# Kernel optimization log

Hardware: AMD Instinct MI355X
Metric: run time of the kernel (lower is better)

Reference implementation:

```python
import jax, jax.numpy as jnp
import numpy as np

B, S, H, D = 1, 2048, 16, 128
CAUSAL = True


def setup_inputs() -> dict:
    key = jax.random.key(0)
    kq, kk, kv = jax.random.split(key, 3)
    query = jax.random.normal(kq, (B, S, H, D), dtype=jnp.float32)
    k_ = jax.random.normal(kk, (B, S, H, D), dtype=jnp.float32)
    v_ = jax.random.normal(kv, (B, S, H, D), dtype=jnp.float32)
    return {"query": query, "key": k_, "value": v_}


def reference(query, key, value):
    # Single-device equivalent of LongContextAttention:
    # Ulysses all-to-all and ring pass are identity on one rank; the math is
    # standard scaled-dot-product attention with flash-attn's default scale
    # softmax_scale = 1/sqrt(head_dim) and causal masking.
    d = query.shape[-1]
    scale = 1.0 / jnp.sqrt(jnp.asarray(d, dtype=query.dtype))
    # [B,S,H,D] x [B,T,H,D] -> [B,H,S,T]
    scores = jnp.einsum("bshd,bthd->bhst", query, key) * scale
    if CAUSAL:
        s, t = scores.shape[-2], scores.shape[-1]
        mask = jnp.tril(jnp.ones((s, t), dtype=bool))
        scores = jnp.where(mask, scores, jnp.finfo(scores.dtype).min)
    probs = jax.nn.softmax(scores, axis=-1)
    out = jnp.einsum("bhst,bthd->bshd", probs, value)
    return out
```

## Files before the change

### kernel.cpp

```cpp
#include <hip/hip_runtime.h>
#include <hip/hip_bf16.h>
#include <math.h>

#define SS 2048
#define HH 16
#define DD 128
#define HD (HH*DD)
#define QBLK 64
#define KVBLK 64

typedef __attribute__((ext_vector_type(8))) short bf16x8;
typedef __attribute__((ext_vector_type(4))) float f32x4;

#if __has_builtin(__builtin_amdgcn_exp2f)
#define EXP2(x) __builtin_amdgcn_exp2f(x)
#else
#define EXP2(x) exp2f(x)
#endif

__device__ __forceinline__ ushort f2bf(float f) {
  __hip_bfloat16 h = __float2bfloat16(f);
  return __builtin_bit_cast(ushort, h);
}

__global__ __launch_bounds__(256, 2)
void attn_fwd(const float* __restrict__ Q, const float* __restrict__ K,
              const float* __restrict__ V, float* __restrict__ O) {
  __shared__ alignas(16) ushort Klds[KVBLK][136];
  __shared__ alignas(16) ushort VTlds[DD][72];
  __shared__ alignas(16) ushort Plds[4][16][72];

  const int tid  = threadIdx.x;
  const int lane = tid & 63;
  const int wid  = tid >> 6;
  const int n    = lane & 15;
  const int g    = lane >> 4;

  const int h  = blockIdx.x & (HH - 1);
  const int j  = blockIdx.x >> 4;
  const int qt = (j < 16) ? (31 - j) : (j - 16);
  const int qb = qt * QBLK;
  const int qw = qb + 16 * wid;

  const float SCALE = 1.44269504088896f / sqrtf((float)DD);

  bf16x8 qfrag[4];
  {
    const float* qrow = Q + ((size_t)(qw + n) * HH + h) * DD;
    #pragma unroll
    for (int ks = 0; ks < 4; ++ks) {
      const int d0 = 32 * ks + 8 * g;
      float4 x = *(const float4*)&qrow[d0];
      float4 y = *(const float4*)&qrow[d0 + 4];
      bf16x8 a;
      a[0] = (short)f2bf(x.x * SCALE); a[1] = (short)f2bf(x.y * SCALE);
      a[2] = (short)f2bf(x.z * SCALE); a[3] = (short)f2bf(x.w * SCALE);
      a[4] = (short)f2bf(y.x * SCALE); a[5] = (short)f2bf(y.y * SCALE);
      a[6] = (short)f2bf(y.z * SCALE); a[7] = (short)f2bf(y.w * SCALE);
      qfrag[ks] = a;
    }
  }

  f32x4 acc[8];
  #pragma unroll
  for (int d0 = 0; d0 < 8; ++d0) { acc[d0][0]=0.f; acc[d0][1]=0.f; acc[d0][2]=0.f; acc[d0][3]=0.f; }
  float m[4] = { -INFINITY, -INFINITY, -INFINITY, -INFINITY };
  float l[4] = { 0.f, 0.f, 0.f, 0.f };

  const float* Kbase = K + (size_t)h * DD;
  const float* Vbase = V + (size_t)h * DD;
  const int nt = qb / KVBLK + 1;

  float4 kreg[8];
  float4 vreg[8];

  {
    #pragma unroll
    for (int it = 0; it < 8; ++it) {
      int li = tid + it * 256;
      int t  = li >> 5;
      int c4 = (li & 31) << 2;
      kreg[it] = *(const float4*)&Kbase[(size_t)t * HD + c4];
    }
    const int dd0 = wid * 16 + n;
    #pragma unroll
    for (int half = 0; half < 2; ++half) {
      #pragma unroll
      for (int jj = 0; jj < 4; ++jj) {
        const float* vp = &Vbase[(size_t)(16 * jj + 4 * g) * HD + (dd0 + 64 * half)];
        vreg[half * 4 + jj] = make_float4(vp[0], vp[HD], vp[2 * HD], vp[3 * HD]);
      }
    }
  }

  for (int itile = 0; itile < nt; ++itile) {
    __syncthreads();

    #pragma unroll
    for (int it = 0; it < 8; ++it) {
      int li = tid + it * 256;
      int t  = li >> 5;
      int c4 = (li & 31) << 2;
      float4 x = kreg[it];
      ushort4 w;
      w.x = f2bf(x.x); w.y = f2bf(x.y); w.z = f2bf(x.z); w.w = f2bf(x.w);
      *(ushort4*)&Klds[t][c4] = w;
    }
    {
      const int dd0 = wid * 16 + n;
      #pragma unroll
      for (int half = 0; half < 2; ++half) {
        #pragma unroll
        for (int jj = 0; jj < 4; ++jj) {
          float4 x = vreg[half * 4 + jj];
          ushort4 w;
          w.x = f2bf(x.x); w.y = f2bf(x.y); w.z = f2bf(x.z); w.w = f2bf(x.w);
          *(ushort4*)&VTlds[dd0 + 64 * half][16 * jj + 4 * g] = w;
        }
      }
    }
    __syncthreads();

    if (itile + 1 < nt) {
      const int t0n = (itile + 1) * KVBLK;
      #pragma unroll
      for (int it = 0; it < 8; ++it) {
        int li = tid + it * 256;
        int t  = li >> 5;
        int c4 = (li & 31) << 2;
        kreg[it] = *(const float4*)&Kbase[(size_t)(t0n + t) * HD + c4];
      }
      const int dd0 = wid * 16 + n;
      #pragma unroll
      for (int half = 0; half < 2; ++half) {
        #pragma unroll
        for (int jj = 0; jj < 4; ++jj) {
          const float* vp = &Vbase[(size_t)(t0n + 16 * jj + 4 * g) * HD + (dd0 + 64 * half)];
          vreg[half * 4 + jj] = make_float4(vp[0], vp[HD], vp[2 * HD], vp[3 * HD]);
        }
      }
    }

    const int t0 = itile * KVBLK;

    f32x4 s[4];
    #pragma unroll
    for (int sub = 0; sub < 4; ++sub) { s[sub][0]=0.f; s[sub][1]=0.f; s[sub][2]=0.f; s[sub][3]=0.f; }
    #pragma unroll
    for (int ks = 0; ks < 4; ++ks) {
      #pragma unroll
      for (int sub = 0; sub < 4; ++sub) {
        bf16x8 b = *(const bf16x8*)&Klds[sub * 16 + n][32 * ks + 8 * g];
        s[sub] = __builtin_amdgcn_mfma_f32_16x16x32_bf16(qfrag[ks], b, s[sub], 0, 0, 0);
      }
    }

    if (t0 + KVBLK - 1 > qw) {
      #pragma unroll
      for (int sub = 0; sub < 4; ++sub) {
        int tg = t0 + sub * 16 + n;
        #pragma unroll
        for (int r = 0; r < 4; ++r) {
          int qg = qw + 4 * g + r;
          if (tg > qg) s[sub][r] = -INFINITY;
        }
      }
    }

    float mr[4];
    #pragma unroll
    for (int r = 0; r < 4; ++r)
      mr[r] = fmaxf(fmaxf(s[0][r], s[1][r]), fmaxf(s[2][r], s[3][r]));
    #pragma unroll
    for (int off = 1; off <= 8; off <<= 1) {
      #pragma unroll
      for (int r = 0; r < 4; ++r)
        mr[r] = fmaxf(mr[r], __shfl_xor(mr[r], off));
    }
    float corr[4];
    #pragma unroll
    for (int r = 0; r < 4; ++r) {
      float mn = fmaxf(m[r], mr[r]);
      corr[r] = EXP2(m[r] - mn);
      m[r] = mn;
    }
    float sr[4] = { 0.f, 0.f, 0.f, 0.f };
    #pragma unroll
    for (int sub = 0; sub < 4; ++sub) {
      #pragma unroll
      for (int r = 0; r < 4; ++r) {
        float p = EXP2(s[sub][r] - m[r]);
        sr[r] += p;
        Plds[wid][4 * g + r][sub * 16 + n] = f2bf(p);
      }
    }
    #pragma unroll
    for (int off = 1; off <= 8; off <<= 1) {
      #pragma unroll
      for (int r = 0; r < 4; ++r)
        sr[r] += __shfl_xor(sr[r], off);
    }
    #pragma unroll
    for (int r = 0; r < 4; ++r) l[r] = l[r] * corr[r] + sr[r];
    #pragma unroll
    for (int d0 = 0; d0 < 8; ++d0) {
      #pragma unroll
      for (int r = 0; r < 4; ++r) acc[d0][r] *= corr[r];
    }

    #pragma unroll
    for (int ks = 0; ks < 2; ++ks) {
      bf16x8 a = *(const bf16x8*)&Plds[wid][n][32 * ks + 8 * g];
      #pragma unroll
      for (int d0 = 0; d0 < 8; ++d0) {
        bf16x8 b = *(const bf16x8*)&VTlds[d0 * 16 + n][32 * ks + 8 * g];
        acc[d0] = __builtin_amdgcn_mfma_f32_16x16x32_bf16(a, b, acc[d0], 0, 0, 0);
      }
    }
  }

  float invl[4];
  #pragma unroll
  for (int r = 0; r < 4; ++r) invl[r] = 1.0f / l[r];
  #pragma unroll
  for (int d0 = 0; d0 < 8; ++d0) {
    #pragma unroll
    for (int r = 0; r < 4; ++r) {
      O[((size_t)(qw + 4 * g + r) * HH + h) * DD + d0 * 16 + n] = acc[d0][r] * invl[r];
    }
  }
}

extern "C" void kernel_launch(void* const* d_in, const int* in_sizes, int n_in,
                              void* d_out, int out_size, void* d_ws, size_t ws_size,
                              hipStream_t stream) {
  const float* Q = (const float*)d_in[0];
  const float* K = (const float*)d_in[1];
  const float* V = (const float*)d_in[2];
  float* O = (float*)d_out;
  dim3 grid((SS / QBLK) * HH);
  attn_fwd<<<grid, 256, 0, stream>>>(Q, K, V, O);
}
```

Before: 75.90 us.

## Split causal attention KV range into chunks with partial outputs and combine kernel

Splits each query tile's KV loop into chunks of at most 8 tiles, so the partial kernel runs more, shorter-lived blocks (1280 tasks) with more even load. Per-chunk unnormalized outputs, row max and row sum go to workspace, and a second kernel merges them with log-sum-exp weights. The goal is to cut the causal load-imbalance tail and raise occupancy, at the cost of a second launch and extra global traffic for the partial outputs. The exp2 intrinsic is also swapped for plain exp2f, and the old single kernel is kept as a fallback when the workspace is too small.

```diff
diff --git a/kernel.cpp b/kernel.cpp
--- a/kernel.cpp
+++ b/kernel.cpp
@@ -8,24 +8,24 @@
 #define HD (HH*DD)
 #define QBLK 64
 #define KVBLK 64
+#define CH 8
+#define NTASK_PER_H 80
+#define NTASK (NTASK_PER_H*HH)
 
 typedef __attribute__((ext_vector_type(8))) short bf16x8;
 typedef __attribute__((ext_vector_type(4))) float f32x4;
 
-#if __has_builtin(__builtin_amdgcn_exp2f)
-#define EXP2(x) __builtin_amdgcn_exp2f(x)
-#else
 #define EXP2(x) exp2f(x)
-#endif
 
 __device__ __forceinline__ ushort f2bf(float f) {
   __hip_bfloat16 h = __float2bfloat16(f);
   return __builtin_bit_cast(ushort, h);
 }
 
-__global__ __launch_bounds__(256, 2)
-void attn_fwd(const float* __restrict__ Q, const float* __restrict__ K,
-              const float* __restrict__ V, float* __restrict__ O) {
+__global__ __launch_bounds__(256, 3)
+void attn_partial(const float* __restrict__ Q, const float* __restrict__ K,
+                  const float* __restrict__ V, float* __restrict__ PO,
+                  float* __restrict__ PM, float* __restrict__ PL) {
   __shared__ alignas(16) ushort Klds[KVBLK][136];
   __shared__ alignas(16) ushort VTlds[DD][72];
   __shared__ alignas(16) ushort Plds[4][16][72];
@@ -36,11 +36,22 @@
   const int n    = lane & 15;
   const int g    = lane >> 4;
 
-  const int h  = blockIdx.x & (HH - 1);
-  const int j  = blockIdx.x >> 4;
-  const int qt = (j < 16) ? (31 - j) : (j - 16);
+  const int bx   = blockIdx.x;
+  const int h    = bx & 15;
+  const int task = bx >> 4;
+
+  int qt = 0, c = 0;
+  for (int q = 31; q >= 0; --q) {
+    int a = q >> 3, b = q & 7;
+    int base = q + 4 * a * (a - 1) + a * b;
+    if (task >= base) { qt = q; c = task - base; break; }
+  }
+
   const int qb = qt * QBLK;
   const int qw = qb + 16 * wid;
+  const int nt = qb / KVBLK + 1;
+  const int tile_lo = c * CH;
+  const int tile_hi = min(tile_lo + CH, nt);
 
   const float SCALE = 1.44269504088896f / sqrtf((float)DD);
 
@@ -69,31 +80,31 @@
 
   const float* Kbase = K + (size_t)h * DD;
   const float* Vbase = V + (size_t)h * DD;
-  const int nt = qb / KVBLK + 1;
 
   float4 kreg[8];
   float4 vreg[8];
 
   {
+    const int t0 = tile_lo * KVBLK;
     #pragma unroll
     for (int it = 0; it < 8; ++it) {
       int li = tid + it * 256;
       int t  = li >> 5;
       int c4 = (li & 31) << 2;
-      kreg[it] = *(const float4*)&Kbase[(size_t)t * HD + c4];
+      kreg[it] = *(const float4*)&Kbase[(size_t)(t0 + t) * HD + c4];
     }
     const int dd0 = wid * 16 + n;
     #pragma unroll
     for (int half = 0; half < 2; ++half) {
       #pragma unroll
       for (int jj = 0; jj < 4; ++jj) {
-        const float* vp = &Vbase[(size_t)(16 * jj + 4 * g) * HD + (dd0 + 64 * half)];
+        const float* vp = &Vbase[(size_t)(t0 + 16 * jj + 4 * g) * HD + (dd0 + 64 * half)];
         vreg[half * 4 + jj] = make_float4(vp[0], vp[HD], vp[2 * HD], vp[3 * HD]);
       }
     }
   }
 
-  for (int itile = 0; itile < nt; ++itile) {
+  for (int itile = tile_lo; itile < tile_hi; ++itile) {
     __syncthreads();
 
     #pragma unroll
@@ -121,7 +132,7 @@
     }
     __syncthreads();
 
-    if (itile + 1 < nt) {
+    if (itile + 1 < tile_hi) {
       const int t0n = (itile + 1) * KVBLK;
       #pragma unroll
       for (int it = 0; it < 8; ++it) {
@@ -219,6 +230,259 @@
     }
   }
 
+  float* po = PO + (size_t)bx * (QBLK * DD);
+  #pragma unroll
+  for (int d0 = 0; d0 < 8; ++d0) {
+    #pragma unroll
+    for (int r = 0; r < 4; ++r) {
+      po[(16 * wid + 4 * g + r) * DD + d0 * 16 + n] = acc[d0][r];
+    }
+  }
+  if (n == 0) {
+    #pragma unroll
+    for (int r = 0; r < 4; ++r) {
+      PM[(size_t)bx * QBLK + 16 * wid + 4 * g + r] = m[r];
+      PL[(size_t)bx * QBLK + 16 * wid + 4 * g + r] = l[r];
+    }
+  }
+}
+
+__global__ __launch_bounds__(256, 4)
+void attn_combine(const float* __restrict__ PO, const float* __restrict__ PM,
+                  const float* __restrict__ PL, float* __restrict__ O) {
+  const int bx = blockIdx.x;
+  const int h  = bx & 15;
+  const int qt = bx >> 4;
+  const int tid = threadIdx.x;
+  const int r  = tid >> 2;
+  const int d0 = (tid & 3) << 5;
+
+  const int a = qt >> 3, b = qt & 7;
+  const int base = qt + 4 * a * (a - 1) + a * b;
+  const int nc = a + 1;
+
+  float mc[4], lc[4];
+  float M = -INFINITY;
+  for (int cc = 0; cc < nc; ++cc) {
+    int pid = ((base + cc) << 4) | h;
+    mc[cc] = PM[(size_t)pid * QBLK + r];
+    lc[cc] = PL[(size_t)pid * QBLK + r];
+    M = fmaxf(M, mc[cc]);
+  }
+  float L = 0.f;
+  float4 o[8];
+  #pragma unroll
+  for (int k = 0; k < 8; ++k) o[k] = make_float4(0.f, 0.f, 0.f, 0.f);
+  for (int cc = 0; cc < nc; ++cc) {
+    int pid = ((base + cc) << 4) | h;
+    float w = EXP2(mc[cc] - M);
+    L += lc[cc] * w;
+    const float* po = PO + (size_t)pid * (QBLK * DD) + r * DD + d0;
+    #pragma unroll
+    for (int k = 0; k < 8; ++k) {
+      float4 x = *(const float4*)&po[4 * k];
+      o[k].x += x.x * w; o[k].y += x.y * w; o[k].z += x.z * w; o[k].w += x.w * w;
+    }
+  }
+  float inv = 1.0f / L;
+  float* op = O + ((size_t)(qt * QBLK + r) * HH + h) * DD + d0;
+  #pragma unroll
+  for (int k = 0; k < 8; ++k) {
+    float4 x = make_float4(o[k].x * inv, o[k].y * inv, o[k].z * inv, o[k].w * inv);
+    *(float4*)&op[4 * k] = x;
+  }
+}
+
+__global__ __launch_bounds__(256, 2)
+void attn_fwd(const float* __restrict__ Q, const float* __restrict__ K,
+              const float* __restrict__ V, float* __restrict__ O) {
+  __shared__ alignas(16) ushort Klds[KVBLK][136];
+  __shared__ alignas(16) ushort VTlds[DD][72];
+  __shared__ alignas(16) ushort Plds[4][16][72];
+
+  const int tid  = threadIdx.x;
+  const int lane = tid & 63;
+  const int wid  = tid >> 6;
+  const int n    = lane & 15;
+  const int g    = lane >> 4;
+
+  const int h  = blockIdx.x & (HH - 1);
+  const int j  = blockIdx.x >> 4;
+  const int qt = (j < 16) ? (31 - j) : (j - 16);
+  const int qb = qt * QBLK;
+  const int qw = qb + 16 * wid;
+
+  const float SCALE = 1.44269504088896f / sqrtf((float)DD);
+
+  bf16x8 qfrag[4];
+  {
+    const float* qrow = Q + ((size_t)(qw + n) * HH + h) * DD;
+    #pragma unroll
+    for (int ks = 0; ks < 4; ++ks) {
+      const int d0 = 32 * ks + 8 * g;
+      float4 x = *(const float4*)&qrow[d0];
+      float4 y = *(const float4*)&qrow[d0 + 4];
+      bf16x8 a;
+      a[0] = (short)f2bf(x.x * SCALE); a[1] = (short)f2bf(x.y * SCALE);
+      a[2] = (short)f2bf(x.z * SCALE); a[3] = (short)f2bf(x.w * SCALE);
+      a[4] = (short)f2bf(y.x * SCALE); a[5] = (short)f2bf(y.y * SCALE);
+      a[6] = (short)f2bf(y.z * SCALE); a[7] = (short)f2bf(y.w * SCALE);
+      qfrag[ks] = a;
+    }
+  }
+
+  f32x4 acc[8];
+  #pragma unroll
+  for (int d0 = 0; d0 < 8; ++d0) { acc[d0][0]=0.f; acc[d0][1]=0.f; acc[d0][2]=0.f; acc[d0][3]=0.f; }
+  float m[4] = { -INFINITY, -INFINITY, -INFINITY, -INFINITY };
+  float l[4] = { 0.f, 0.f, 0.f, 0.f };
+
+  const float* Kbase = K + (size_t)h * DD;
+  const float* Vbase = V + (size_t)h * DD;
+  const int nt = qb / KVBLK + 1;
+
+  float4 kreg[8];
+  float4 vreg[8];
+  {
+    #pragma unroll
+    for (int it = 0; it < 8; ++it) {
+      int li = tid + it * 256;
+      int t  = li >> 5;
+      int c4 = (li & 31) << 2;
+      kreg[it] = *(const float4*)&Kbase[(size_t)t * HD + c4];
+    }
+    const int dd0 = wid * 16 + n;
+    #pragma unroll
+    for (int half = 0; half < 2; ++half) {
+      #pragma unroll
+      for (int jj = 0; jj < 4; ++jj) {
+        const float* vp = &Vbase[(size_t)(16 * jj + 4 * g) * HD + (dd0 + 64 * half)];
+        vreg[half * 4 + jj] = make_float4(vp[0], vp[HD], vp[2 * HD], vp[3 * HD]);
+      }
+    }
+  }
+
+  for (int itile = 0; itile < nt; ++itile) {
+    __syncthreads();
+    #pragma unroll
+    for (int it = 0; it < 8; ++it) {
+      int li = tid + it * 256;
+      int t  = li >> 5;
+      int c4 = (li & 31) << 2;
+      float4 x = kreg[it];
+      ushort4 w;
+      w.x = f2bf(x.x); w.y = f2bf(x.y); w.z = f2bf(x.z); w.w = f2bf(x.w);
+      *(ushort4*)&Klds[t][c4] = w;
+    }
+    {
+      const int dd0 = wid * 16 + n;
+      #pragma unroll
+      for (int half = 0; half < 2; ++half) {
+        #pragma unroll
+        for (int jj = 0; jj < 4; ++jj) {
+          float4 x = vreg[half * 4 + jj];
+          ushort4 w;
+          w.x = f2bf(x.x); w.y = f2bf(x.y); w.z = f2bf(x.z); w.w = f2bf(x.w);
+          *(ushort4*)&VTlds[dd0 + 64 * half][16 * jj + 4 * g] = w;
+        }
+      }
+    }
+    __syncthreads();
+
+    if (itile + 1 < nt) {
+      const int t0n = (itile + 1) * KVBLK;
+      #pragma unroll
+      for (int it = 0; it < 8; ++it) {
+        int li = tid + it * 256;
+        int t  = li >> 5;
+        int c4 = (li & 31) << 2;
+        kreg[it] = *(const float4*)&Kbase[(size_t)(t0n + t) * HD + c4];
+      }
+      const int dd0 = wid * 16 + n;
+      #pragma unroll
+      for (int half = 0; half < 2; ++half) {
+        #pragma unroll
+        for (int jj = 0; jj < 4; ++jj) {
+          const float* vp = &Vbase[(size_t)(t0n + 16 * jj + 4 * g) * HD + (dd0 + 64 * half)];
+          vreg[half * 4 + jj] = make_float4(vp[0], vp[HD], vp[2 * HD], vp[3 * HD]);
+        }
+      }
+    }
+
+    const int t0 = itile * KVBLK;
+    f32x4 s[4];
+    #pragma unroll
+    for (int sub = 0; sub < 4; ++sub) { s[sub][0]=0.f; s[sub][1]=0.f; s[sub][2]=0.f; s[sub][3]=0.f; }
+    #pragma unroll
+    for (int ks = 0; ks < 4; ++ks) {
+      #pragma unroll
+      for (int sub = 0; sub < 4; ++sub) {
+        bf16x8 b = *(const bf16x8*)&Klds[sub * 16 + n][32 * ks + 8 * g];
+        s[sub] = __builtin_amdgcn_mfma_f32_16x16x32_bf16(qfrag[ks], b, s[sub], 0, 0, 0);
+      }
+    }
+    if (t0 + KVBLK - 1 > qw) {
+      #pragma unroll
+      for (int sub = 0; sub < 4; ++sub) {
+        int tg = t0 + sub * 16 + n;
+        #pragma unroll
+        for (int r = 0; r < 4; ++r) {
+          int qg = qw + 4 * g + r;
+          if (tg > qg) s[sub][r] = -INFINITY;
+        }
+      }
+    }
+    float mr[4];
+    #pragma unroll
+    for (int r = 0; r < 4; ++r)
+      mr[r] = fmaxf(fmaxf(s[0][r], s[1][r]), fmaxf(s[2][r], s[3][r]));
+    #pragma unroll
+    for (int off = 1; off <= 8; off <<= 1) {
+      #pragma unroll
+      for (int r = 0; r < 4; ++r)
+        mr[r] = fmaxf(mr[r], __shfl_xor(mr[r], off));
+    }
+    float corr[4];
+    #pragma unroll
+    for (int r = 0; r < 4; ++r) {
+      float mn = fmaxf(m[r], mr[r]);
+      corr[r] = EXP2(m[r] - mn);
+      m[r] = mn;
+    }
+    float sr[4] = { 0.f, 0.f, 0.f, 0.f };
+    #pragma unroll
+    for (int sub = 0; sub < 4; ++sub) {
+      #pragma unroll
+      for (int r = 0; r < 4; ++r) {
+        float p = EXP2(s[sub][r] - m[r]);
+        sr[r] += p;
+        Plds[wid][4 * g + r][sub * 16 + n] = f2bf(p);
+      }
+    }
+    #pragma unroll
+    for (int off = 1; off <= 8; off <<= 1) {
+      #pragma unroll
+      for (int r = 0; r < 4; ++r)
+        sr[r] += __shfl_xor(sr[r], off);
+    }
+    #pragma unroll
+    for (int r = 0; r < 4; ++r) l[r] = l[r] * corr[r] + sr[r];
+    #pragma unroll
+    for (int d0 = 0; d0 < 8; ++d0) {
+      #pragma unroll
+      for (int r = 0; r < 4; ++r) acc[d0][r] *= corr[r];
+    }
+    #pragma unroll
+    for (int ks = 0; ks < 2; ++ks) {
+      bf16x8 a = *(const bf16x8*)&Plds[wid][n][32 * ks + 8 * g];
+      #pragma unroll
+      for (int d0 = 0; d0 < 8; ++d0) {
+        bf16x8 b = *(const bf16x8*)&VTlds[d0 * 16 + n][32 * ks + 8 * g];
+        acc[d0] = __builtin_amdgcn_mfma_f32_16x16x32_bf16(a, b, acc[d0], 0, 0, 0);
+      }
+    }
+  }
+
   float invl[4];
   #pragma unroll
   for (int r = 0; r < 4; ++r) invl[r] = 1.0f / l[r];
@@ -238,6 +502,18 @@
   const float* K = (const float*)d_in[1];
   const float* V = (const float*)d_in[2];
   float* O = (float*)d_out;
-  dim3 grid((SS / QBLK) * HH);
-  attn_fwd<<<grid, 256, 0, stream>>>(Q, K, V, O);
+
+  const size_t po_elems = (size_t)NTASK * QBLK * DD;
+  const size_t ml_elems = (size_t)NTASK * QBLK;
+  const size_t ws_needed = (po_elems + 2 * ml_elems) * sizeof(float);
+
+  if (ws_size >= ws_needed) {
+    float* PO = (float*)d_ws;
+    float* PM = PO + po_elems;
+    float* PL = PM + ml_elems;
+    attn_partial<<<NTASK, 256, 0, stream>>>(Q, K, V, PO, PM, PL);
+    attn_combine<<<(SS / QBLK) * HH, 256, 0, stream>>>(PO, PM, PL, O);
+  } else {
+    attn_fwd<<<(SS / QBLK) * HH, 256, 0, stream>>>(Q, K, V, O);
+  }
 }
```

New measurement: 116.9 us. 1.54x slower.

## Precompute bf16 K and transposed V in a prep kernel, swizzle LDS

Applied to the files above, without the earlier changes.

Adds a prep kernel that converts K to bf16 and V to a transposed bf16 layout in workspace once per call. The attention kernel then streams half-size bf16 tiles with contiguous 16-byte loads instead of redoing the fp32 conversion and strided V gathers in every query block. LDS tiles lose their padding and use an XOR swizzle to avoid bank conflicts, and launch bounds rise to 3 blocks per CU. The cost is an extra kernel launch plus a workspace round trip. The exp2 macro is also switched from the amdgcn builtin to exp2f.

```diff
diff --git a/kernel.cpp b/kernel.cpp
--- a/kernel.cpp
+++ b/kernel.cpp
@@ -12,22 +12,73 @@
 typedef __attribute__((ext_vector_type(8))) short bf16x8;
 typedef __attribute__((ext_vector_type(4))) float f32x4;
 
-#if __has_builtin(__builtin_amdgcn_exp2f)
-#define EXP2(x) __builtin_amdgcn_exp2f(x)
-#else
 #define EXP2(x) exp2f(x)
-#endif
 
 __device__ __forceinline__ ushort f2bf(float f) {
   __hip_bfloat16 h = __float2bfloat16(f);
   return __builtin_bit_cast(ushort, h);
 }
 
-__global__ __launch_bounds__(256, 2)
-void attn_fwd(const float* __restrict__ Q, const float* __restrict__ K,
-              const float* __restrict__ V, float* __restrict__ O) {
-  __shared__ alignas(16) ushort Klds[KVBLK][136];
-  __shared__ alignas(16) ushort VTlds[DD][72];
+__global__ __launch_bounds__(256, 4)
+void prep_kv(const float* __restrict__ K, const float* __restrict__ V,
+             ushort* __restrict__ Kbf, ushort* __restrict__ VTg) {
+  __shared__ ushort Vlds[64][136];
+  const int tid = threadIdx.x;
+  const int h  = blockIdx.x & 15;
+  const int t0 = (blockIdx.x >> 4) * 64;
+
+  #pragma unroll
+  for (int j = 0; j < 2; ++j) {
+    int li = tid + j * 256;
+    int t  = li >> 3;
+    int c  = (li & 7) << 4;
+    const float* src = K + ((size_t)(t0 + t) * HH + h) * DD + c;
+    ushort tmp[16];
+    #pragma unroll
+    for (int q = 0; q < 4; ++q) {
+      float4 x = *(const float4*)(src + 4 * q);
+      tmp[4*q+0] = f2bf(x.x); tmp[4*q+1] = f2bf(x.y);
+      tmp[4*q+2] = f2bf(x.z); tmp[4*q+3] = f2bf(x.w);
+    }
+    ushort* dst = Kbf + ((size_t)h * SS + t0 + t) * DD + c;
+    *(uint4*)dst       = *(uint4*)&tmp[0];
+    *(uint4*)(dst + 8) = *(uint4*)&tmp[8];
+  }
+
+  #pragma unroll
+  for (int j = 0; j < 2; ++j) {
+    int li = tid + j * 256;
+    int t  = li >> 3;
+    int c  = (li & 7) << 4;
+    const float* src = V + ((size_t)(t0 + t) * HH + h) * DD + c;
+    #pragma unroll
+    for (int q = 0; q < 4; ++q) {
+      float4 x = *(const float4*)(src + 4 * q);
+      ushort4 w; w.x = f2bf(x.x); w.y = f2bf(x.y); w.z = f2bf(x.z); w.w = f2bf(x.w);
+      *(ushort4*)&Vlds[t][c + 4 * q] = w;
+    }
+  }
+  __syncthreads();
+
+  #pragma unroll
+  for (int j = 0; j < 2; ++j) {
+    int li  = tid + j * 256;
+    int d   = li >> 2;
+    int t16 = (li & 3) << 4;
+    ushort tmp[16];
+    #pragma unroll
+    for (int k = 0; k < 16; ++k) tmp[k] = Vlds[t16 + k][d];
+    ushort* dst = VTg + ((size_t)h * DD + d) * SS + t0 + t16;
+    *(uint4*)dst       = *(uint4*)&tmp[0];
+    *(uint4*)(dst + 8) = *(uint4*)&tmp[8];
+  }
+}
+
+__global__ __launch_bounds__(256, 3)
+void attn_fwd(const float* __restrict__ Q, const ushort* __restrict__ Kbf,
+              const ushort* __restrict__ VTg, float* __restrict__ O) {
+  __shared__ alignas(16) ushort Klds[KVBLK * DD];
+  __shared__ alignas(16) ushort VTlds[DD * KVBLK];
   __shared__ alignas(16) ushort Plds[4][16][72];
 
   const int tid  = threadIdx.x;
@@ -35,6 +86,7 @@
   const int wid  = tid >> 6;
   const int n    = lane & 15;
   const int g    = lane >> 4;
+  const int kx   = (n & 7) << 4;
 
   const int h  = blockIdx.x & (HH - 1);
   const int j  = blockIdx.x >> 4;
@@ -67,77 +119,40 @@
   float m[4] = { -INFINITY, -INFINITY, -INFINITY, -INFINITY };
   float l[4] = { 0.f, 0.f, 0.f, 0.f };
 
-  const float* Kbase = K + (size_t)h * DD;
-  const float* Vbase = V + (size_t)h * DD;
+  const ushort* Kh  = Kbf + (size_t)h * SS * DD;
+  const ushort* VTh = VTg + (size_t)h * DD * SS;
   const int nt = qb / KVBLK + 1;
 
-  float4 kreg[8];
-  float4 vreg[8];
-
-  {
-    #pragma unroll
-    for (int it = 0; it < 8; ++it) {
-      int li = tid + it * 256;
-      int t  = li >> 5;
-      int c4 = (li & 31) << 2;
-      kreg[it] = *(const float4*)&Kbase[(size_t)t * HD + c4];
-    }
-    const int dd0 = wid * 16 + n;
-    #pragma unroll
-    for (int half = 0; half < 2; ++half) {
-      #pragma unroll
-      for (int jj = 0; jj < 4; ++jj) {
-        const float* vp = &Vbase[(size_t)(16 * jj + 4 * g) * HD + (dd0 + 64 * half)];
-        vreg[half * 4 + jj] = make_float4(vp[0], vp[HD], vp[2 * HD], vp[3 * HD]);
-      }
-    }
+  uint4 kreg[4], vreg[4];
+
+  #pragma unroll
+  for (int it = 0; it < 4; ++it) {
+    int e = (tid + it * 256) * 8;
+    kreg[it] = *(const uint4*)(Kh + e);
+    int d = e >> 6, c = e & 63;
+    vreg[it] = *(const uint4*)(VTh + (size_t)d * SS + c);
   }
 
   for (int itile = 0; itile < nt; ++itile) {
     __syncthreads();
 
     #pragma unroll
-    for (int it = 0; it < 8; ++it) {
-      int li = tid + it * 256;
-      int t  = li >> 5;
-      int c4 = (li & 31) << 2;
-      float4 x = kreg[it];
-      ushort4 w;
-      w.x = f2bf(x.x); w.y = f2bf(x.y); w.z = f2bf(x.z); w.w = f2bf(x.w);
-      *(ushort4*)&Klds[t][c4] = w;
-    }
-    {
-      const int dd0 = wid * 16 + n;
-      #pragma unroll
-      for (int half = 0; half < 2; ++half) {
-        #pragma unroll
-        for (int jj = 0; jj < 4; ++jj) {
-          float4 x = vreg[half * 4 + jj];
-          ushort4 w;
-          w.x = f2bf(x.x); w.y = f2bf(x.y); w.z = f2bf(x.z); w.w = f2bf(x.w);
-          *(ushort4*)&VTlds[dd0 + 64 * half][16 * jj + 4 * g] = w;
-        }
-      }
+    for (int it = 0; it < 4; ++it) {
+      int e  = (tid + it * 256) * 8;
+      int by = 2 * e;
+      *(uint4*)((char*)Klds  + (by ^ (((e >> 7) & 7) << 4))) = kreg[it];
+      *(uint4*)((char*)VTlds + (by ^ (((e >> 6) & 7) << 4))) = vreg[it];
     }
     __syncthreads();
 
     if (itile + 1 < nt) {
       const int t0n = (itile + 1) * KVBLK;
       #pragma unroll
-      for (int it = 0; it < 8; ++it) {
-        int li = tid + it * 256;
-        int t  = li >> 5;
-        int c4 = (li & 31) << 2;
-        kreg[it] = *(const float4*)&Kbase[(size_t)(t0n + t) * HD + c4];
-      }
-      const int dd0 = wid * 16 + n;
-      #pragma unroll
-      for (int half = 0; half < 2; ++half) {
-        #pragma unroll
-        for (int jj = 0; jj < 4; ++jj) {
-          const float* vp = &Vbase[(size_t)(t0n + 16 * jj + 4 * g) * HD + (dd0 + 64 * half)];
-          vreg[half * 4 + jj] = make_float4(vp[0], vp[HD], vp[2 * HD], vp[3 * HD]);
-        }
+      for (int it = 0; it < 4; ++it) {
+        int e = (tid + it * 256) * 8;
+        kreg[it] = *(const uint4*)(Kh + (size_t)t0n * DD + e);
+        int d = e >> 6, c = e & 63;
+        vreg[it] = *(const uint4*)(VTh + (size_t)d * SS + t0n + c);
       }
     }
 
@@ -150,7 +165,8 @@
     for (int ks = 0; ks < 4; ++ks) {
       #pragma unroll
       for (int sub = 0; sub < 4; ++sub) {
-        bf16x8 b = *(const bf16x8*)&Klds[sub * 16 + n][32 * ks + 8 * g];
+        bf16x8 b = *(const bf16x8*)((const char*)Klds +
+                     (sub * 16 + n) * 256 + ((64 * ks + 16 * g) ^ kx));
         s[sub] = __builtin_amdgcn_mfma_f32_16x16x32_bf16(qfrag[ks], b, s[sub], 0, 0, 0);
       }
     }
@@ -213,7 +229,8 @@
       bf16x8 a = *(const bf16x8*)&Plds[wid][n][32 * ks + 8 * g];
       #pragma unroll
       for (int d0 = 0; d0 < 8; ++d0) {
-        bf16x8 b = *(const bf16x8*)&VTlds[d0 * 16 + n][32 * ks + 8 * g];
+        bf16x8 b = *(const bf16x8*)((const char*)VTlds +
+                     (d0 * 16 + n) * 128 + ((64 * ks + 16 * g) ^ kx));
         acc[d0] = __builtin_amdgcn_mfma_f32_16x16x32_bf16(a, b, acc[d0], 0, 0, 0);
       }
     }
@@ -238,6 +255,11 @@
   const float* K = (const float*)d_in[1];
   const float* V = (const float*)d_in[2];
   float* O = (float*)d_out;
-  dim3 grid((SS / QBLK) * HH);
-  attn_fwd<<<grid, 256, 0, stream>>>(Q, K, V, O);
-}
+
+  const size_t kv_elems = (size_t)HH * SS * DD;
+  ushort* Kbf = (ushort*)d_ws;
+  ushort* VTg = Kbf + kv_elems;
+
+  prep_kv<<<dim3(HH * (SS / 64)), 256, 0, stream>>>(K, V, Kbf, VTg);
+  attn_fwd<<<dim3((SS / QBLK) * HH), 256, 0, stream>>>(Q, Kbf, VTg, O);
+}
```

After: 130.2 us. 71.5% more time.

## Split long causal query tiles across two blocks and merge partials

Applied to the files above, without the earlier changes.

Rebalances causal work by having each block handle one short query tile plus the first half of a long tile. A second block handles the remaining half of the long tile. The partial outputs, max and sum are written to workspace, and a new merge kernel combines them, a split-KV flash-decoding style scheme. This evens out per-block work across 512 equally loaded blocks. In exchange it adds a second kernel launch, extra global traffic for the partials, and a switch from the amdgcn exp2 builtin to exp2f.

```diff
diff --git a/kernel.cpp b/kernel.cpp
--- a/kernel.cpp
+++ b/kernel.cpp
@@ -12,20 +12,40 @@
 typedef __attribute__((ext_vector_type(8))) short bf16x8;
 typedef __attribute__((ext_vector_type(4))) float f32x4;
 
-#if __has_builtin(__builtin_amdgcn_exp2f)
-#define EXP2(x) __builtin_amdgcn_exp2f(x)
-#else
 #define EXP2(x) exp2f(x)
-#endif
 
 __device__ __forceinline__ ushort f2bf(float f) {
   __hip_bfloat16 h = __float2bfloat16(f);
   return __builtin_bit_cast(ushort, h);
 }
 
+__device__ __forceinline__ void prefetch_tile(const float* __restrict__ Kbase,
+                                              const float* __restrict__ Vbase,
+                                              int t0, int tid, int wid, int n, int g,
+                                              float4* kreg, float4* vreg) {
+  #pragma unroll
+  for (int it = 0; it < 8; ++it) {
+    int li = tid + it * 256;
+    int t  = li >> 5;
+    int c4 = (li & 31) << 2;
+    kreg[it] = *(const float4*)&Kbase[(size_t)(t0 + t) * HD + c4];
+  }
+  const int dd0 = wid * 16 + n;
+  #pragma unroll
+  for (int half = 0; half < 2; ++half) {
+    #pragma unroll
+    for (int jj = 0; jj < 4; ++jj) {
+      const float* vp = &Vbase[(size_t)(t0 + 16 * jj + 4 * g) * HD + (dd0 + 64 * half)];
+      vreg[half * 4 + jj] = make_float4(vp[0], vp[HD], vp[2 * HD], vp[3 * HD]);
+    }
+  }
+}
+
 __global__ __launch_bounds__(256, 2)
 void attn_fwd(const float* __restrict__ Q, const float* __restrict__ K,
-              const float* __restrict__ V, float* __restrict__ O) {
+              const float* __restrict__ V, float* __restrict__ O,
+              float* __restrict__ PO, float* __restrict__ PM,
+              float* __restrict__ PL) {
   __shared__ alignas(16) ushort Klds[KVBLK][136];
   __shared__ alignas(16) ushort VTlds[DD][72];
   __shared__ alignas(16) ushort Plds[4][16][72];
@@ -36,198 +56,228 @@
   const int n    = lane & 15;
   const int g    = lane >> 4;
 
-  const int h  = blockIdx.x & (HH - 1);
-  const int j  = blockIdx.x >> 4;
-  const int qt = (j < 16) ? (31 - j) : (j - 16);
-  const int qb = qt * QBLK;
-  const int qw = qb + 16 * wid;
+  const int h     = blockIdx.x & (HH - 1);
+  const int job   = blockIdx.x >> 4;
+  const int p     = job & 15;
+  const int which = job >> 4;
 
   const float SCALE = 1.44269504088896f / sqrtf((float)DD);
-
-  bf16x8 qfrag[4];
-  {
-    const float* qrow = Q + ((size_t)(qw + n) * HH + h) * DD;
-    #pragma unroll
-    for (int ks = 0; ks < 4; ++ks) {
-      const int d0 = 32 * ks + 8 * g;
-      float4 x = *(const float4*)&qrow[d0];
-      float4 y = *(const float4*)&qrow[d0 + 4];
-      bf16x8 a;
-      a[0] = (short)f2bf(x.x * SCALE); a[1] = (short)f2bf(x.y * SCALE);
-      a[2] = (short)f2bf(x.z * SCALE); a[3] = (short)f2bf(x.w * SCALE);
-      a[4] = (short)f2bf(y.x * SCALE); a[5] = (short)f2bf(y.y * SCALE);
-      a[6] = (short)f2bf(y.z * SCALE); a[7] = (short)f2bf(y.w * SCALE);
-      qfrag[ks] = a;
-    }
-  }
-
-  f32x4 acc[8];
-  #pragma unroll
-  for (int d0 = 0; d0 < 8; ++d0) { acc[d0][0]=0.f; acc[d0][1]=0.f; acc[d0][2]=0.f; acc[d0][3]=0.f; }
-  float m[4] = { -INFINITY, -INFINITY, -INFINITY, -INFINITY };
-  float l[4] = { 0.f, 0.f, 0.f, 0.f };
-
   const float* Kbase = K + (size_t)h * DD;
   const float* Vbase = V + (size_t)h * DD;
-  const int nt = qb / KVBLK + 1;
-
-  float4 kreg[8];
-  float4 vreg[8];
-
-  {
+
+  const int nph = (which == 0) ? 2 : 1;
+
+  for (int ph = 0; ph < nph; ++ph) {
+    int qt_, lo, hi, fin, slot;
+    if (which == 0) {
+      if (ph == 0) { qt_ = p;      lo = 0;      hi = p + 1;  fin = 1; slot = 0; }
+      else         { qt_ = 31 - p; lo = 0;      hi = 16 - p; fin = 0; slot = 0; }
+    } else         { qt_ = 31 - p; lo = 16 - p; hi = 32 - p; fin = 0; slot = 1; }
+
+    const int qb = qt_ * QBLK;
+    const int qw = qb + 16 * wid;
+
+    bf16x8 qfrag[4];
+    {
+      const float* qrow = Q + ((size_t)(qw + n) * HH + h) * DD;
+      #pragma unroll
+      for (int ks = 0; ks < 4; ++ks) {
+        const int d0 = 32 * ks + 8 * g;
+        float4 x = *(const float4*)&qrow[d0];
+        float4 y = *(const float4*)&qrow[d0 + 4];
+        bf16x8 a;
+        a[0] = (short)f2bf(x.x * SCALE); a[1] = (short)f2bf(x.y * SCALE);
+        a[2] = (short)f2bf(x.z * SCALE); a[3] = (short)f2bf(x.w * SCALE);
+        a[4] = (short)f2bf(y.x * SCALE); a[5] = (short)f2bf(y.y * SCALE);
+        a[6] = (short)f2bf(y.z * SCALE); a[7] = (short)f2bf(y.w * SCALE);
+        qfrag[ks] = a;
+      }
+    }
+
+    f32x4 acc[8];
     #pragma unroll
-    for (int it = 0; it < 8; ++it) {
-      int li = tid + it * 256;
-      int t  = li >> 5;
-      int c4 = (li & 31) << 2;
-      kreg[it] = *(const float4*)&Kbase[(size_t)t * HD + c4];
-    }
-    const int dd0 = wid * 16 + n;
-    #pragma unroll
-    for (int half = 0; half < 2; ++half) {
-      #pragma unroll
-      for (int jj = 0; jj < 4; ++jj) {
-        const float* vp = &Vbase[(size_t)(16 * jj + 4 * g) * HD + (dd0 + 64 * half)];
-        vreg[half * 4 + jj] = make_float4(vp[0], vp[HD], vp[2 * HD], vp[3 * HD]);
-      }
-    }
-  }
-
-  for (int itile = 0; itile < nt; ++itile) {
-    __syncthreads();
-
-    #pragma unroll
-    for (int it = 0; it < 8; ++it) {
-      int li = tid + it * 256;
-      int t  = li >> 5;
-      int c4 = (li & 31) << 2;
-      float4 x = kreg[it];
-      ushort4 w;
-      w.x = f2bf(x.x); w.y = f2bf(x.y); w.z = f2bf(x.z); w.w = f2bf(x.w);
-      *(ushort4*)&Klds[t][c4] = w;
-    }
-    {
-      const int dd0 = wid * 16 + n;
-      #pragma unroll
-      for (int half = 0; half < 2; ++half) {
-        #pragma unroll
-        for (int jj = 0; jj < 4; ++jj) {
-          float4 x = vreg[half * 4 + jj];
-          ushort4 w;
-          w.x = f2bf(x.x); w.y = f2bf(x.y); w.z = f2bf(x.z); w.w = f2bf(x.w);
-          *(ushort4*)&VTlds[dd0 + 64 * half][16 * jj + 4 * g] = w;
-        }
-      }
-    }
-    __syncthreads();
-
-    if (itile + 1 < nt) {
-      const int t0n = (itile + 1) * KVBLK;
+    for (int d0 = 0; d0 < 8; ++d0) { acc[d0][0]=0.f; acc[d0][1]=0.f; acc[d0][2]=0.f; acc[d0][3]=0.f; }
+    float m[4] = { -INFINITY, -INFINITY, -INFINITY, -INFINITY };
+    float l[4] = { 0.f, 0.f, 0.f, 0.f };
+
+    float4 kreg[8], vreg[8];
+    prefetch_tile(Kbase, Vbase, lo * KVBLK, tid, wid, n, g, kreg, vreg);
+
+    for (int itile = lo; itile < hi; ++itile) {
+      __syncthreads();
+
       #pragma unroll
       for (int it = 0; it < 8; ++it) {
         int li = tid + it * 256;
         int t  = li >> 5;
         int c4 = (li & 31) << 2;
-        kreg[it] = *(const float4*)&Kbase[(size_t)(t0n + t) * HD + c4];
-      }
-      const int dd0 = wid * 16 + n;
-      #pragma unroll
-      for (int half = 0; half < 2; ++half) {
-        #pragma unroll
-        for (int jj = 0; jj < 4; ++jj) {
-          const float* vp = &Vbase[(size_t)(t0n + 16 * jj + 4 * g) * HD + (dd0 + 64 * half)];
-          vreg[half * 4 + jj] = make_float4(vp[0], vp[HD], vp[2 * HD], vp[3 * HD]);
+        float4 x = kreg[it];
+        ushort4 w;
+        w.x = f2bf(x.x); w.y = f2bf(x.y); w.z = f2bf(x.z); w.w = f2bf(x.w);
+        *(ushort4*)&Klds[t][c4] = w;
+      }
+      {
+        const int dd0 = wid * 16 + n;
+        #pragma unroll
+        for (int half = 0; half < 2; ++half) {
+          #pragma unroll
+          for (int jj = 0; jj < 4; ++jj) {
+            float4 x = vreg[half * 4 + jj];
+            ushort4 w;
+            w.x = f2bf(x.x); w.y = f2bf(x.y); w.z = f2bf(x.z); w.w = f2bf(x.w);
+            *(ushort4*)&VTlds[dd0 + 64 * half][16 * jj + 4 * g] = w;
+          }
+        }
+      }
+      __syncthreads();
+
+      if (itile + 1 < hi) {
+        prefetch_tile(Kbase, Vbase, (itile + 1) * KVBLK, tid, wid, n, g, kreg, vreg);
+      }
+
+      const int t0 = itile * KVBLK;
+
+      f32x4 s[4];
+      #pragma unroll
+      for (int sub = 0; sub < 4; ++sub) { s[sub][0]=0.f; s[sub][1]=0.f; s[sub][2]=0.f; s[sub][3]=0.f; }
+      #pragma unroll
+      for (int ks = 0; ks < 4; ++ks) {
+        #pragma unroll
+        for (int sub = 0; sub < 4; ++sub) {
+          bf16x8 b = *(const bf16x8*)&Klds[sub * 16 + n][32 * ks + 8 * g];
+          s[sub] = __builtin_amdgcn_mfma_f32_16x16x32_bf16(qfrag[ks], b, s[sub], 0, 0, 0);
+        }
+      }
+
+      if (t0 + KVBLK - 1 > qw) {
+        #pragma unroll
+        for (int sub = 0; sub < 4; ++sub) {
+          int tg = t0 + sub * 16 + n;
+          #pragma unroll
+          for (int r = 0; r < 4; ++r) {
+            int qg = qw + 4 * g + r;
+            if (tg > qg) s[sub][r] = -INFINITY;
+          }
+        }
+      }
+
+      float mr[4];
+      #pragma unroll
+      for (int r = 0; r < 4; ++r)
+        mr[r] = fmaxf(fmaxf(s[0][r], s[1][r]), fmaxf(s[2][r], s[3][r]));
+      #pragma unroll
+      for (int off = 1; off <= 8; off <<= 1) {
+        #pragma unroll
+        for (int r = 0; r < 4; ++r)
+          mr[r] = fmaxf(mr[r], __shfl_xor(mr[r], off));
+      }
+      float corr[4];
+      #pragma unroll
+      for (int r = 0; r < 4; ++r) {
+        float mn = fmaxf(m[r], mr[r]);
+        corr[r] = EXP2(m[r] - mn);
+        m[r] = mn;
+      }
+      float sr[4] = { 0.f, 0.f, 0.f, 0.f };
+      #pragma unroll
+      for (int sub = 0; sub < 4; ++sub) {
+        #pragma unroll
+        for (int r = 0; r < 4; ++r) {
+          float pp = EXP2(s[sub][r] - m[r]);
+          sr[r] += pp;
+          Plds[wid][4 * g + r][sub * 16 + n] = f2bf(pp);
+        }
+      }
+      #pragma unroll
+      for (int off = 1; off <= 8; off <<= 1) {
+        #pragma unroll
+        for (int r = 0; r < 4; ++r)
+          sr[r] += __shfl_xor(sr[r], off);
+      }
+      #pragma unroll
+      for (int r = 0; r < 4; ++r) l[r] = l[r] * corr[r] + sr[r];
+      #pragma unroll
+      for (int d0 = 0; d0 < 8; ++d0) {
+        #pragma unroll
+        for (int r = 0; r < 4; ++r) acc[d0][r] *= corr[r];
+      }
+
+      #pragma unroll
+      for (int ks = 0; ks < 2; ++ks) {
+        bf16x8 a = *(const bf16x8*)&Plds[wid][n][32 * ks + 8 * g];
+        #pragma unroll
+        for (int d0 = 0; d0 < 8; ++d0) {
+          bf16x8 b = *(const bf16x8*)&VTlds[d0 * 16 + n][32 * ks + 8 * g];
+          acc[d0] = __builtin_amdgcn_mfma_f32_16x16x32_bf16(a, b, acc[d0], 0, 0, 0);
         }
       }
     }
 
-    const int t0 = itile * KVBLK;
-
-    f32x4 s[4];
-    #pragma unroll
-    for (int sub = 0; sub < 4; ++sub) { s[sub][0]=0.f; s[sub][1]=0.f; s[sub][2]=0.f; s[sub][3]=0.f; }
-    #pragma unroll
-    for (int ks = 0; ks < 4; ++ks) {
-      #pragma unroll
-      for (int sub = 0; sub < 4; ++sub) {
-        bf16x8 b = *(const bf16x8*)&Klds[sub * 16 + n][32 * ks + 8 * g];
-        s[sub] = __builtin_amdgcn_mfma_f32_16x16x32_bf16(qfrag[ks], b, s[sub], 0, 0, 0);
-      }
-    }
-
-    if (t0 + KVBLK - 1 > qw) {
-      #pragma unroll
-      for (int sub = 0; sub < 4; ++sub) {
-        int tg = t0 + sub * 16 + n;
+    if (fin) {
+      float invl[4];
+      #pragma unroll
+      for (int r = 0; r < 4; ++r) invl[r] = 1.0f / l[r];
+      #pragma unroll
+      for (int d0 = 0; d0 < 8; ++d0) {
         #pragma unroll
         for (int r = 0; r < 4; ++r) {
-          int qg = qw + 4 * g + r;
-          if (tg > qg) s[sub][r] = -INFINITY;
-        }
-      }
-    }
-
-    float mr[4];
-    #pragma unroll
-    for (int r = 0; r < 4; ++r)
-      mr[r] = fmaxf(fmaxf(s[0][r], s[1][r]), fmaxf(s[2][r], s[3][r]));
-    #pragma unroll
-    for (int off = 1; off <= 8; off <<= 1) {
-      #pragma unroll
-      for (int r = 0; r < 4; ++r)
-        mr[r] = fmaxf(mr[r], __shfl_xor(mr[r], off));
-    }
-    float corr[4];
-    #pragma unroll
-    for (int r = 0; r < 4; ++r) {
-      float mn = fmaxf(m[r], mr[r]);
-      corr[r] = EXP2(m[r] - mn);
-      m[r] = mn;
-    }
-    float sr[4] = { 0.f, 0.f, 0.f, 0.f };
-    #pragma unroll
-    for (int sub = 0; sub < 4; ++sub) {
-      #pragma unroll
-      for (int r = 0; r < 4; ++r) {
-        float p = EXP2(s[sub][r] - m[r]);
-        sr[r] += p;
-        Plds[wid][4 * g + r][sub * 16 + n] = f2bf(p);
-      }
-    }
-    #pragma unroll
-    for (int off = 1; off <= 8; off <<= 1) {
-      #pragma unroll
-      for (int r = 0; r < 4; ++r)
-        sr[r] += __shfl_xor(sr[r], off);
-    }
-    #pragma unroll
-    for (int r = 0; r < 4; ++r) l[r] = l[r] * corr[r] + sr[r];
-    #pragma unroll
-    for (int d0 = 0; d0 < 8; ++d0) {
-      #pragma unroll
-      for (int r = 0; r < 4; ++r) acc[d0][r] *= corr[r];
-    }
-
-    #pragma unroll
-    for (int ks = 0; ks < 2; ++ks) {
-      bf16x8 a = *(const bf16x8*)&Plds[wid][n][32 * ks + 8 * g];
+          O[((size_t)(qw + 4 * g + r) * HH + h) * DD + d0 * 16 + n] = acc[d0][r] * invl[r];
+        }
+      }
+    } else {
+      const int pidx = (h * 16 + (qt_ - 16)) * 2 + slot;
+      float* po = PO + (size_t)pidx * (QBLK * DD);
       #pragma unroll
       for (int d0 = 0; d0 < 8; ++d0) {
-        bf16x8 b = *(const bf16x8*)&VTlds[d0 * 16 + n][32 * ks + 8 * g];
-        acc[d0] = __builtin_amdgcn_mfma_f32_16x16x32_bf16(a, b, acc[d0], 0, 0, 0);
+        #pragma unroll
+        for (int r = 0; r < 4; ++r) {
+          po[(16 * wid + 4 * g + r) * DD + d0 * 16 + n] = acc[d0][r];
+        }
+      }
+      if (n == 0) {
+        #pragma unroll
+        for (int r = 0; r < 4; ++r) {
+          PM[(size_t)pidx * QBLK + 16 * wid + 4 * g + r] = m[r];
+          PL[(size_t)pidx * QBLK + 16 * wid + 4 * g + r] = l[r];
+        }
       }
     }
   }
-
-  float invl[4];
+}
+
+__global__ __launch_bounds__(256, 8)
+void attn_merge(const float* __restrict__ PO, const float* __restrict__ PM,
+                const float* __restrict__ PL, float* __restrict__ O) {
+  const int bx  = blockIdx.x;
+  const int h   = bx & 15;
+  const int qtb = bx >> 4;
+  const int qt  = 16 + qtb;
+  const int tid = threadIdx.x;
+  const int r   = tid >> 2;
+  const int dc  = (tid & 3) << 5;
+
+  const int i0 = (h * 16 + qtb) * 2;
+  const int i1 = i0 + 1;
+  float m0 = PM[(size_t)i0 * QBLK + r], m1 = PM[(size_t)i1 * QBLK + r];
+  float l0 = PL[(size_t)i0 * QBLK + r], l1 = PL[(size_t)i1 * QBLK + r];
+  float M  = fmaxf(m0, m1);
+  float w0 = EXP2(m0 - M), w1 = EXP2(m1 - M);
+  float inv = 1.0f / (l0 * w0 + l1 * w1);
+  w0 *= inv; w1 *= inv;
+
+  const float* a = PO + (size_t)i0 * (QBLK * DD) + r * DD + dc;
+  const float* b = PO + (size_t)i1 * (QBLK * DD) + r * DD + dc;
+  float* op = O + ((size_t)(qt * QBLK + r) * HH + h) * DD + dc;
   #pragma unroll
-  for (int r = 0; r < 4; ++r) invl[r] = 1.0f / l[r];
-  #pragma unroll
-  for (int d0 = 0; d0 < 8; ++d0) {
-    #pragma unroll
-    for (int r = 0; r < 4; ++r) {
-      O[((size_t)(qw + 4 * g + r) * HH + h) * DD + d0 * 16 + n] = acc[d0][r] * invl[r];
-    }
+  for (int k = 0; k < 8; ++k) {
+    float4 x = *(const float4*)&a[4 * k];
+    float4 y = *(const float4*)&b[4 * k];
+    float4 o;
+    o.x = x.x * w0 + y.x * w1;
+    o.y = x.y * w0 + y.y * w1;
+    o.z = x.z * w0 + y.z * w1;
+    o.w = x.w * w0 + y.w * w1;
+    *(float4*)&op[4 * k] = o;
   }
 }
 
@@ -238,6 +288,13 @@
   const float* K = (const float*)d_in[1];
   const float* V = (const float*)d_in[2];
   float* O = (float*)d_out;
-  dim3 grid((SS / QBLK) * HH);
-  attn_fwd<<<grid, 256, 0, stream>>>(Q, K, V, O);
-}
+
+  const size_t po_elems = (size_t)512 * QBLK * DD;
+  const size_t ml_elems = (size_t)512 * QBLK;
+  float* PO = (float*)d_ws;
+  float* PM = PO + po_elems;
+  float* PL = PM + ml_elems;
+
+  attn_fwd<<<dim3(512), 256, 0, stream>>>(Q, K, V, O, PO, PM, PL);
+  attn_merge<<<dim3(256), 256, 0, stream>>>(PO, PM, PL, O);
+}
```

New measurement: 78.78 us. +3.8%, slower.
